# Performance work log

Hardware: AMD Instinct MI355X
Metric: run time of the kernel (lower is better)

The kernel has to match this reference:

```python
import jax, jax.numpy as jnp
import numpy as np

D_MODEL = 768
HEAD_SIZE = 64

def setup_inputs() -> dict:
    key = jax.random.key(0)
    ks = jax.random.split(key, 7)
    B, S = 8, 2048
    x = jax.random.normal(ks[0], (B, S, D_MODEL), dtype=jnp.float32)
    s = 1.0 / np.sqrt(D_MODEL)
    Wq = jax.random.uniform(ks[1], (D_MODEL, HEAD_SIZE), jnp.float32, -s, s)
    bq = jnp.zeros((HEAD_SIZE,), jnp.float32)
    Wk = jax.random.uniform(ks[2], (D_MODEL, HEAD_SIZE), jnp.float32, -s, s)
    bk = jnp.zeros((HEAD_SIZE,), jnp.float32)
    Wv = jax.random.uniform(ks[3], (D_MODEL, HEAD_SIZE), jnp.float32, -s, s)
    bv = jnp.zeros((HEAD_SIZE,), jnp.float32)
    return {"x": x, "Wq": Wq, "bq": bq, "Wk": Wk, "bk": bk, "Wv": Wv, "bv": bv}

def reference(x, Wq, bq, Wk, bk, Wv, bv):
    # Single attention head: softmax(Q K^T / sqrt(head_size)) V
    q = jnp.einsum('bsd,dh->bsh', x, Wq) + bq  # [B,S,H]
    k = jnp.einsum('bsd,dh->bsh', x, Wk) + bk
    v = jnp.einsum('bsd,dh->bsh', x, Wv) + bv
    scale = 1.0 / jnp.sqrt(jnp.array(HEAD_SIZE, dtype=x.dtype))
    scores = jnp.einsum('bqh,bkh->bqk', q, k) * scale  # [B,S,S]
    attn = jax.nn.softmax(scores, axis=-1)
    out = jnp.einsum('bqk,bkh->bqh', attn, v)  # [B,S,H]
    return out
```

## Files before the change

kernel.cpp:

```cpp
#include <hip/hip_runtime.h>
#include <math.h>

#define D_MODEL 768
#define HS 64
#define BATCH 8
#define SEQ 2048
#define SCALE 0.125f

typedef _Float16 half_t;
typedef __attribute__((ext_vector_type(8))) _Float16 half8;
typedef __attribute__((ext_vector_type(4))) float floatx4;

__global__ __launch_bounds__(256)
void wconv_kernel(const float* __restrict__ Wq, const float* __restrict__ Wk,
                  const float* __restrict__ Wv, half_t* __restrict__ Wt)
{
    int m = blockIdx.x >> 6;
    int h = blockIdx.x & 63;
    const float* W = (m == 0) ? Wq : ((m == 1) ? Wk : Wv);
    half_t* dst = Wt + (size_t)blockIdx.x * D_MODEL;
    for (int k = threadIdx.x; k < D_MODEL; k += 256)
        dst[k] = (half_t)W[(size_t)k * HS + h];
}

__global__ __launch_bounds__(256)
void proj_kernel(const float* __restrict__ x, const half_t* __restrict__ Wt,
                 const float* __restrict__ bq, const float* __restrict__ bk,
                 const float* __restrict__ bv,
                 half_t* __restrict__ Qh, half_t* __restrict__ Kh,
                 half_t* __restrict__ Vt)
{
    __shared__ __align__(16) float  xs[2][32 * 64];
    __shared__ __align__(16) half_t wt[2][192 * 64];

    const int tid = threadIdx.x;
    const int w = tid >> 6;
    const int lane = tid & 63;
    const int l15 = lane & 15;
    const int quad = lane >> 4;
    const long row0 = (long)blockIdx.x * 32;

    floatx4 acc[2][3];
#pragma unroll
    for (int i = 0; i < 2; ++i)
#pragma unroll
        for (int j = 0; j < 3; ++j) acc[i][j] = (floatx4){0.f, 0.f, 0.f, 0.f};

    float4 xA[2], xB[2];
    half8  wA[6], wB[6];

    auto loadx = [&](int k0, float4 (&xr)[2]) {
#pragma unroll
        for (int i = 0; i < 2; ++i) {
            int idx = i * 256 + tid;
            int r = idx >> 4, sc = idx & 15;
            int cg = sc ^ (r & 15);
            xr[i] = *(const float4*)(x + (row0 + r) * D_MODEL + k0 + cg * 4);
        }
    };
    auto loadw = [&](int k0, half8 (&wr)[6]) {
#pragma unroll
        for (int i = 0; i < 6; ++i) {
            int idx = i * 256 + tid;
            int r = idx >> 3, sc = idx & 7;
            int cg = sc ^ (r & 7);
            wr[i] = *(const half8*)(Wt + (size_t)r * D_MODEL + k0 + cg * 8);
        }
    };

    auto step = [&](int it, float4 (&xc)[2], half8 (&wc)[6],
                    float4 (&xn)[2], half8 (&wn)[6], int p) {
#pragma unroll
        for (int i = 0; i < 2; ++i) {
            int idx = i * 256 + tid;
            *(float4*)&xs[p][idx * 4] = xc[i];
        }
#pragma unroll
        for (int i = 0; i < 6; ++i) {
            int idx = i * 256 + tid;
            *(half8*)&wt[p][idx * 8] = wc[i];
        }
        int kn = (it + 1 < 12) ? (it + 1) * 64 : 0;
        loadx(kn, xn);
        loadw(kn, wn);
        __syncthreads();
#pragma unroll
        for (int kst = 0; kst < 2; ++kst) {
            half8 af[2];
#pragma unroll
            for (int mt = 0; mt < 2; ++mt) {
                int r = mt * 16 + l15;
                int c0 = kst * 8 + quad * 2;
                float4 f0 = *(const float4*)&xs[p][r * 64 + (c0 ^ l15) * 4];
                float4 f1 = *(const float4*)&xs[p][r * 64 + ((c0 + 1) ^ l15) * 4];
                af[mt] = (half8){(half_t)f0.x, (half_t)f0.y, (half_t)f0.z, (half_t)f0.w,
                                 (half_t)f1.x, (half_t)f1.y, (half_t)f1.z, (half_t)f1.w};
            }
#pragma unroll
            for (int nt = 0; nt < 3; ++nt) {
                int r = w * 48 + nt * 16 + l15;
                int slot = (kst * 4 + quad) ^ (r & 7);
                half8 bf = *(const half8*)&wt[p][r * 64 + slot * 8];
#pragma unroll
                for (int mt = 0; mt < 2; ++mt)
                    acc[mt][nt] = __builtin_amdgcn_mfma_f32_16x16x32_f16(
                        af[mt], bf, acc[mt][nt], 0, 0, 0);
            }
        }
    };

    loadx(0, xA);
    loadw(0, wA);
#pragma unroll
    for (int it = 0; it < 12; it += 2) {
        step(it,     xA, wA, xB, wB, 0);
        step(it + 1, xB, wB, xA, wA, 1);
    }

#pragma unroll
    for (int nt = 0; nt < 3; ++nt) {
        int nbase = w * 48 + nt * 16;
        int mm = nbase >> 6;
        int h = (nbase + l15) & 63;
        const float* bias = (mm == 0) ? bq : ((mm == 1) ? bk : bv);
        float bval = bias[h];
#pragma unroll
        for (int mt = 0; mt < 2; ++mt)
#pragma unroll
            for (int r = 0; r < 4; ++r) {
                long R = row0 + mt * 16 + quad * 4 + r;
                half_t hv = (half_t)(acc[mt][nt][r] + bval);
                if (mm == 0)      Qh[R * HS + h] = hv;
                else if (mm == 1) Kh[R * HS + h] = hv;
                else {
                    long b = R >> 11, s = R & 2047;
                    Vt[(b * HS + h) * SEQ + s] = hv;
                }
            }
    }
}

__global__ __launch_bounds__(256)
void attn_kernel(const half_t* __restrict__ Qh, const half_t* __restrict__ Kh,
                 const half_t* __restrict__ Vt,
                 half_t* __restrict__ Opart, float* __restrict__ lpart,
                 int kchunk)
{
    __shared__ __align__(16) half_t ks[2][64 * 64];
    __shared__ __align__(16) half_t vs[2][64 * 64];
    __shared__ __align__(16) half_t ps[4][32][72];

    const int tid = threadIdx.x;
    const int w = tid >> 6;
    const int lane = tid & 63;
    const int l15 = lane & 15;
    const int quad = lane >> 4;
    const int b = blockIdx.y;
    const int q0 = blockIdx.x * 128 + w * 32;
    const int kh = blockIdx.z;
    const int kk_begin = kh * kchunk;
    const int nk = kchunk >> 6;

    const half_t* Kb = Kh + (size_t)b * SEQ * HS;
    const half_t* Vb = Vt + (size_t)b * HS * SEQ;

    half8 qf[2][2];
#pragma unroll
    for (int mt = 0; mt < 2; ++mt)
#pragma unroll
        for (int kst = 0; kst < 2; ++kst) {
            half8 q = *(const half8*)(Qh + ((size_t)b * SEQ + q0 + mt * 16 + l15) * HS
                                      + kst * 32 + quad * 8);
#pragma unroll
            for (int j = 0; j < 8; ++j) q[j] = q[j] * (half_t)SCALE;
            qf[mt][kst] = q;
        }

    floatx4 oacc[2][4];
    float lsum[2][4];
#pragma unroll
    for (int mt = 0; mt < 2; ++mt) {
#pragma unroll
        for (int nt = 0; nt < 4; ++nt) oacc[mt][nt] = (floatx4){0.f, 0.f, 0.f, 0.f};
#pragma unroll
        for (int r = 0; r < 4; ++r) lsum[mt][r] = 0.f;
    }

    half8 kA[2], vA[2], kB[2], vB[2];

    auto loadkv = [&](int kk0, half8 (&kc)[2], half8 (&vc)[2]) {
#pragma unroll
        for (int i = 0; i < 2; ++i) {
            int idx = i * 256 + tid;
            int r = idx >> 3, sc = idx & 7;
            int cg = sc ^ (r & 7);
            kc[i] = *(const half8*)(Kb + (size_t)(kk0 + r) * HS + cg * 8);
            vc[i] = *(const half8*)(Vb + (size_t)r * SEQ + kk0 + cg * 8);
        }
    };

    auto step = [&](int kkn, half8 (&kc)[2], half8 (&vc)[2],
                    half8 (&kn_)[2], half8 (&vn_)[2], int p) {
#pragma unroll
        for (int i = 0; i < 2; ++i) {
            int idx = i * 256 + tid;
            *(half8*)&ks[p][idx * 8] = kc[i];
            *(half8*)&vs[p][idx * 8] = vc[i];
        }
        loadkv(kkn, kn_, vn_);
        __syncthreads();

        floatx4 sacc[2][4];
#pragma unroll
        for (int mt = 0; mt < 2; ++mt)
#pragma unroll
            for (int nt = 0; nt < 4; ++nt) sacc[mt][nt] = (floatx4){0.f, 0.f, 0.f, 0.f};
#pragma unroll
        for (int nt = 0; nt < 4; ++nt)
#pragma unroll
            for (int kst = 0; kst < 2; ++kst) {
                int r = nt * 16 + l15;
                int slot = (kst * 4 + quad) ^ (r & 7);
                half8 kf = *(const half8*)&ks[p][r * 64 + slot * 8];
#pragma unroll
                for (int mt = 0; mt < 2; ++mt)
                    sacc[mt][nt] = __builtin_amdgcn_mfma_f32_16x16x32_f16(
                        qf[mt][kst], kf, sacc[mt][nt], 0, 0, 0);
            }

#pragma unroll
        for (int mt = 0; mt < 2; ++mt)
#pragma unroll
            for (int nt = 0; nt < 4; ++nt)
#pragma unroll
                for (int r = 0; r < 4; ++r) {
                    float pv = __expf(sacc[mt][nt][r]);
                    lsum[mt][r] += pv;
                    ps[w][mt * 16 + quad * 4 + r][nt * 16 + l15] = (half_t)pv;
                }

        half8 pfr[2][2];
#pragma unroll
        for (int mt = 0; mt < 2; ++mt)
#pragma unroll
            for (int kst = 0; kst < 2; ++kst)
                pfr[mt][kst] = *(const half8*)&ps[w][mt * 16 + l15][kst * 32 + quad * 8];

#pragma unroll
        for (int nt = 0; nt < 4; ++nt)
#pragma unroll
            for (int kst = 0; kst < 2; ++kst) {
                int r = nt * 16 + l15;
                int slot = (kst * 4 + quad) ^ (r & 7);
                half8 vf = *(const half8*)&vs[p][r * 64 + slot * 8];
#pragma unroll
                for (int mt = 0; mt < 2; ++mt)
                    oacc[mt][nt] = __builtin_amdgcn_mfma_f32_16x16x32_f16(
                        pfr[mt][kst], vf, oacc[mt][nt], 0, 0, 0);
            }
    };

    loadkv(kk_begin, kA, vA);
    for (int it = 0; it < nk; it += 2) {
        int kk1 = kk_begin + it * 64 + 64;
        int kk2 = (it + 2 < nk) ? (kk1 + 64) : kk_begin;
        step(kk1, kA, vA, kB, vB, 0);
        step(kk2, kB, vB, kA, vA, 1);
    }

#pragma unroll
    for (int mt = 0; mt < 2; ++mt)
#pragma unroll
        for (int r = 0; r < 4; ++r) {
            float s = lsum[mt][r];
            s += __shfl_xor(s, 1);
            s += __shfl_xor(s, 2);
            s += __shfl_xor(s, 4);
            s += __shfl_xor(s, 8);
            lsum[mt][r] = s;
        }

    size_t obase = ((size_t)kh * BATCH + b) * SEQ * HS;
#pragma unroll
    for (int mt = 0; mt < 2; ++mt)
#pragma unroll
        for (int nt = 0; nt < 4; ++nt)
#pragma unroll
            for (int r = 0; r < 4; ++r) {
                int row = q0 + mt * 16 + quad * 4 + r;
                Opart[obase + (size_t)row * HS + nt * 16 + l15] = (half_t)oacc[mt][nt][r];
            }
    if (l15 == 0) {
#pragma unroll
        for (int mt = 0; mt < 2; ++mt)
#pragma unroll
            for (int r = 0; r < 4; ++r) {
                int row = q0 + mt * 16 + quad * 4 + r;
                lpart[((size_t)kh * BATCH + b) * SEQ + row] = lsum[mt][r];
            }
    }
}

__global__ __launch_bounds__(256)
void combine_kernel(const half_t* __restrict__ Opart, const float* __restrict__ lpart,
                    float* __restrict__ out, int nsplit)
{
    const size_t NT = (size_t)BATCH * SEQ * HS;
    const size_t BS = (size_t)BATCH * SEQ;
    size_t e0 = ((size_t)blockIdx.x * 256 + threadIdx.x) * 8;
    size_t row = e0 / HS;
    float o[8] = {0, 0, 0, 0, 0, 0, 0, 0};
    float l = 0.f;
    for (int i = 0; i < nsplit; ++i) {
        half8 oi = *(const half8*)(Opart + (size_t)i * NT + e0);
#pragma unroll
        for (int j = 0; j < 8; ++j) o[j] += (float)oi[j];
        l += lpart[(size_t)i * BS + row];
    }
    float inv = 1.f / l;
    float4 a = {o[0] * inv, o[1] * inv, o[2] * inv, o[3] * inv};
    float4 c = {o[4] * inv, o[5] * inv, o[6] * inv, o[7] * inv};
    *(float4*)(out + e0) = a;
    *(float4*)(out + e0 + 4) = c;
}

extern "C" void kernel_launch(void* const* d_in, const int* in_sizes, int n_in,
                              void* d_out, int out_size, void* d_ws, size_t ws_size,
                              hipStream_t stream) {
    const float* x  = (const float*)d_in[0];
    const float* Wq = (const float*)d_in[1];
    const float* bq = (const float*)d_in[2];
    const float* Wk = (const float*)d_in[3];
    const float* bk = (const float*)d_in[4];
    const float* Wv = (const float*)d_in[5];
    const float* bv = (const float*)d_in[6];
    float* out = (float*)d_out;

    const size_t per = (size_t)BATCH * SEQ * HS;
    half_t* Qh = (half_t*)d_ws;
    half_t* Kh = Qh + per;
    half_t* Vt = Kh + per;
    half_t* Wt = Vt + per;
    half_t* Opart = Wt + 3 * HS * D_MODEL;
    const size_t base_bytes = (3 * per + 3 * HS * D_MODEL) * sizeof(half_t);
    const size_t split_bytes = per * sizeof(half_t) + (size_t)BATCH * SEQ * sizeof(float);

    int ksplit = 2;
    if (ws_size >= base_bytes + 8 * split_bytes) ksplit = 8;
    else if (ws_size >= base_bytes + 4 * split_bytes) ksplit = 4;
    float* lpart = (float*)(Opart + (size_t)ksplit * per);

    wconv_kernel<<<dim3(3 * HS), dim3(256), 0, stream>>>(Wq, Wk, Wv, Wt);
    proj_kernel<<<dim3(BATCH * SEQ / 32), dim3(256), 0, stream>>>(
        x, Wt, bq, bk, bv, Qh, Kh, Vt);
    attn_kernel<<<dim3(SEQ / 128, BATCH, ksplit), dim3(256), 0, stream>>>(
        Qh, Kh, Vt, Opart, lpart, SEQ / ksplit);
    combine_kernel<<<dim3((BATCH * SEQ * HS) / (256 * 8)), dim3(256), 0, stream>>>(
        Opart, lpart, out, ksplit);
}
```

Baseline: 143.8 us.

## Enlarge attention query tile per wave and store x as fp16 in shared memory

```diff
diff --git a/kernel.cpp b/kernel.cpp
--- a/kernel.cpp
+++ b/kernel.cpp
@@ -30,7 +30,7 @@
                  half_t* __restrict__ Qh, half_t* __restrict__ Kh,
                  half_t* __restrict__ Vt)
 {
-    __shared__ __align__(16) float  xs[2][32 * 64];
+    __shared__ __align__(16) half_t xs[2][32 * 64];
     __shared__ __align__(16) half_t wt[2][192 * 64];
 
     const int tid = threadIdx.x;
@@ -46,17 +46,16 @@
 #pragma unroll
         for (int j = 0; j < 3; ++j) acc[i][j] = (floatx4){0.f, 0.f, 0.f, 0.f};
 
+    const int xr = tid >> 3, xsc = tid & 7;
+    const int xcg = xsc ^ (xr & 7);
+    const float* xaddr = x + (row0 + xr) * D_MODEL + xcg * 8;
+
     float4 xA[2], xB[2];
     half8  wA[6], wB[6];
 
-    auto loadx = [&](int k0, float4 (&xr)[2]) {
-#pragma unroll
-        for (int i = 0; i < 2; ++i) {
-            int idx = i * 256 + tid;
-            int r = idx >> 4, sc = idx & 15;
-            int cg = sc ^ (r & 15);
-            xr[i] = *(const float4*)(x + (row0 + r) * D_MODEL + k0 + cg * 4);
-        }
+    auto loadx = [&](int k0, float4 (&v)[2]) {
+        v[0] = *(const float4*)(xaddr + k0);
+        v[1] = *(const float4*)(xaddr + k0 + 4);
     };
     auto loadw = [&](int k0, half8 (&wr)[6]) {
 #pragma unroll
@@ -70,31 +69,24 @@
 
     auto step = [&](int it, float4 (&xc)[2], half8 (&wc)[6],
                     float4 (&xn)[2], half8 (&wn)[6], int p) {
-#pragma unroll
-        for (int i = 0; i < 2; ++i) {
-            int idx = i * 256 + tid;
-            *(float4*)&xs[p][idx * 4] = xc[i];
-        }
-#pragma unroll
-        for (int i = 0; i < 6; ++i) {
-            int idx = i * 256 + tid;
-            *(half8*)&wt[p][idx * 8] = wc[i];
-        }
+        half8 xh = (half8){(half_t)xc[0].x, (half_t)xc[0].y, (half_t)xc[0].z, (half_t)xc[0].w,
+                           (half_t)xc[1].x, (half_t)xc[1].y, (half_t)xc[1].z, (half_t)xc[1].w};
+        *(half8*)&xs[p][tid * 8] = xh;
+#pragma unroll
+        for (int i = 0; i < 6; ++i)
+            *(half8*)&wt[p][(i * 256 + tid) * 8] = wc[i];
+        __syncthreads();
         int kn = (it + 1 < 12) ? (it + 1) * 64 : 0;
         loadx(kn, xn);
         loadw(kn, wn);
-        __syncthreads();
 #pragma unroll
         for (int kst = 0; kst < 2; ++kst) {
             half8 af[2];
 #pragma unroll
             for (int mt = 0; mt < 2; ++mt) {
                 int r = mt * 16 + l15;
-                int c0 = kst * 8 + quad * 2;
-                float4 f0 = *(const float4*)&xs[p][r * 64 + (c0 ^ l15) * 4];
-                float4 f1 = *(const float4*)&xs[p][r * 64 + ((c0 + 1) ^ l15) * 4];
-                af[mt] = (half8){(half_t)f0.x, (half_t)f0.y, (half_t)f0.z, (half_t)f0.w,
-                                 (half_t)f1.x, (half_t)f1.y, (half_t)f1.z, (half_t)f1.w};
+                int slot = (kst * 4 + quad) ^ (r & 7);
+                af[mt] = *(const half8*)&xs[p][r * 64 + slot * 8];
             }
 #pragma unroll
             for (int nt = 0; nt < 3; ++nt) {
@@ -156,7 +148,7 @@
     const int l15 = lane & 15;
     const int quad = lane >> 4;
     const int b = blockIdx.y;
-    const int q0 = blockIdx.x * 128 + w * 32;
+    const int q0 = blockIdx.x * 256 + w * 64;
     const int kh = blockIdx.z;
     const int kk_begin = kh * kchunk;
     const int nk = kchunk >> 6;
@@ -164,9 +156,9 @@
     const half_t* Kb = Kh + (size_t)b * SEQ * HS;
     const half_t* Vb = Vt + (size_t)b * HS * SEQ;
 
-    half8 qf[2][2];
-#pragma unroll
-    for (int mt = 0; mt < 2; ++mt)
+    half8 qf[4][2];
+#pragma unroll
+    for (int mt = 0; mt < 4; ++mt)
 #pragma unroll
         for (int kst = 0; kst < 2; ++kst) {
             half8 q = *(const half8*)(Qh + ((size_t)b * SEQ + q0 + mt * 16 + l15) * HS
@@ -176,10 +168,10 @@
             qf[mt][kst] = q;
         }
 
-    floatx4 oacc[2][4];
-    float lsum[2][4];
-#pragma unroll
-    for (int mt = 0; mt < 2; ++mt) {
+    floatx4 oacc[4][4];
+    float lsum[4][4];
+#pragma unroll
+    for (int mt = 0; mt < 4; ++mt) {
 #pragma unroll
         for (int nt = 0; nt < 4; ++nt) oacc[mt][nt] = (floatx4){0.f, 0.f, 0.f, 0.f};
 #pragma unroll
@@ -207,12 +199,12 @@
             *(half8*)&ks[p][idx * 8] = kc[i];
             *(half8*)&vs[p][idx * 8] = vc[i];
         }
+        __syncthreads();
         loadkv(kkn, kn_, vn_);
-        __syncthreads();
-
-        floatx4 sacc[2][4];
-#pragma unroll
-        for (int mt = 0; mt < 2; ++mt)
+
+        floatx4 sacc[4][4];
+#pragma unroll
+        for (int mt = 0; mt < 4; ++mt)
 #pragma unroll
             for (int nt = 0; nt < 4; ++nt) sacc[mt][nt] = (floatx4){0.f, 0.f, 0.f, 0.f};
 #pragma unroll
@@ -223,41 +215,44 @@
                 int slot = (kst * 4 + quad) ^ (r & 7);
                 half8 kf = *(const half8*)&ks[p][r * 64 + slot * 8];
 #pragma unroll
-                for (int mt = 0; mt < 2; ++mt)
+                for (int mt = 0; mt < 4; ++mt)
                     sacc[mt][nt] = __builtin_amdgcn_mfma_f32_16x16x32_f16(
                         qf[mt][kst], kf, sacc[mt][nt], 0, 0, 0);
             }
 
 #pragma unroll
-        for (int mt = 0; mt < 2; ++mt)
+        for (int h2 = 0; h2 < 2; ++h2) {
+#pragma unroll
+            for (int mtl = 0; mtl < 2; ++mtl) {
+                int mt = h2 * 2 + mtl;
+#pragma unroll
+                for (int nt = 0; nt < 4; ++nt)
+#pragma unroll
+                    for (int r = 0; r < 4; ++r) {
+                        float pv = __expf(sacc[mt][nt][r]);
+                        lsum[mt][r] += pv;
+                        ps[w][mtl * 16 + quad * 4 + r][nt * 16 + l15] = (half_t)pv;
+                    }
+            }
+            half8 pfr[2][2];
+#pragma unroll
+            for (int mtl = 0; mtl < 2; ++mtl)
+#pragma unroll
+                for (int kst = 0; kst < 2; ++kst)
+                    pfr[mtl][kst] = *(const half8*)&ps[w][mtl * 16 + l15][kst * 32 + quad * 8];
 #pragma unroll
             for (int nt = 0; nt < 4; ++nt)
 #pragma unroll
-                for (int r = 0; r < 4; ++r) {
-                    float pv = __expf(sacc[mt][nt][r]);
-                    lsum[mt][r] += pv;
-                    ps[w][mt * 16 + quad * 4 + r][nt * 16 + l15] = (half_t)pv;
+                for (int kst = 0; kst < 2; ++kst) {
+                    int r = nt * 16 + l15;
+                    int slot = (kst * 4 + quad) ^ (r & 7);
+                    half8 vf = *(const half8*)&vs[p][r * 64 + slot * 8];
+#pragma unroll
+                    for (int mtl = 0; mtl < 2; ++mtl)
+                        oacc[h2 * 2 + mtl][nt] = __builtin_amdgcn_mfma_f32_16x16x32_f16(
+                            pfr[mtl][kst], vf, oacc[h2 * 2 + mtl][nt], 0, 0, 0);
                 }
-
-        half8 pfr[2][2];
-#pragma unroll
-        for (int mt = 0; mt < 2; ++mt)
-#pragma unroll
-            for (int kst = 0; kst < 2; ++kst)
-                pfr[mt][kst] = *(const half8*)&ps[w][mt * 16 + l15][kst * 32 + quad * 8];
-
-#pragma unroll
-        for (int nt = 0; nt < 4; ++nt)
-#pragma unroll
-            for (int kst = 0; kst < 2; ++kst) {
-                int r = nt * 16 + l15;
-                int slot = (kst * 4 + quad) ^ (r & 7);
-                half8 vf = *(const half8*)&vs[p][r * 64 + slot * 8];
-#pragma unroll
-                for (int mt = 0; mt < 2; ++mt)
-                    oacc[mt][nt] = __builtin_amdgcn_mfma_f32_16x16x32_f16(
-                        pfr[mt][kst], vf, oacc[mt][nt], 0, 0, 0);
-            }
+        }
     };
 
     loadkv(kk_begin, kA, vA);
@@ -269,7 +264,7 @@
     }
 
 #pragma unroll
-    for (int mt = 0; mt < 2; ++mt)
+    for (int mt = 0; mt < 4; ++mt)
 #pragma unroll
         for (int r = 0; r < 4; ++r) {
             float s = lsum[mt][r];
@@ -282,7 +277,7 @@
 
     size_t obase = ((size_t)kh * BATCH + b) * SEQ * HS;
 #pragma unroll
-    for (int mt = 0; mt < 2; ++mt)
+    for (int mt = 0; mt < 4; ++mt)
 #pragma unroll
         for (int nt = 0; nt < 4; ++nt)
 #pragma unroll
@@ -292,7 +287,7 @@
             }
     if (l15 == 0) {
 #pragma unroll
-        for (int mt = 0; mt < 2; ++mt)
+        for (int mt = 0; mt < 4; ++mt)
 #pragma unroll
             for (int r = 0; r < 4; ++r) {
                 int row = q0 + mt * 16 + quad * 4 + r;
@@ -353,7 +348,7 @@
     wconv_kernel<<<dim3(3 * HS), dim3(256), 0, stream>>>(Wq, Wk, Wv, Wt);
     proj_kernel<<<dim3(BATCH * SEQ / 32), dim3(256), 0, stream>>>(
         x, Wt, bq, bk, bv, Qh, Kh, Vt);
-    attn_kernel<<<dim3(SEQ / 128, BATCH, ksplit), dim3(256), 0, stream>>>(
+    attn_kernel<<<dim3(SEQ / 256, BATCH, ksplit), dim3(256), 0, stream>>>(
         Qh, Kh, Vt, Opart, lpart, SEQ / ksplit);
     combine_kernel<<<dim3((BATCH * SEQ * HS) / (256 * 8)), dim3(256), 0, stream>>>(
         Opart, lpart, out, ksplit);
```

Result: no change. 143.3 us (-0.3%).
